# Kernel optimization log

Measured on AMD Instinct MI355X. Metric: run time of the kernel, lower is better.

Reference implementation:

```python
import jax, jax.numpy as jnp
import numpy as np

BATCH = 4096
NNZ = 32
VOCAB = 1_000_000
DIM = 64


def setup_inputs() -> dict:
    key = jax.random.key(0)
    k1, k2, k3, k4 = jax.random.split(key, 4)
    idx = jax.random.randint(k1, (BATCH, NNZ), 0, VOCAB, dtype=jnp.int32)
    vals = jax.random.uniform(k2, (BATCH, NNZ), dtype=jnp.float32)
    kernel = jax.random.normal(k3, (VOCAB, DIM), dtype=jnp.float32)
    bias = jax.random.normal(k4, (DIM,), dtype=jnp.float32)
    return {"idx": idx, "vals": vals, "kernel": kernel, "bias": bias}


def reference(idx, vals, kernel, bias):
    # Sparse [B, V] x dense [V, D] matmul == weighted gather-sum (embedding bag)
    gathered = kernel[idx]                      # [B, nnz, D] irregular gather
    out = jnp.einsum("bn,bnd->bd", vals, gathered) + bias  # [B, D]
    return out
```

## Files before the change

kernel.cpp:

```cpp
#include <hip/hip_runtime.h>
#include <hip/hip_bf16.h>


#define B_BATCH 4096
#define NNZ 32
#define DIM 64
#define LANES_PER_ROW 16

__global__ __launch_bounds__(256) void sparse_embed_kernel(
    const int* __restrict__ idx,
    const float* __restrict__ vals,
    const float* __restrict__ kern,
    const float* __restrict__ bias,
    float* __restrict__ out)
{
    const int tid  = blockIdx.x * blockDim.x + threadIdx.x;
    const int row  = tid >> 4;
    const int lane = tid & 15;
    if (row >= B_BATCH) return;

    const int*   irow = idx  + row * NNZ;
    const float* vrow = vals + row * NNZ;

    float4 acc = make_float4(0.f, 0.f, 0.f, 0.f);

    #pragma unroll
    for (int n = 0; n < NNZ; ++n) {
        const int   id = irow[n];
        const float v  = vrow[n];
        const float4 k = *reinterpret_cast<const float4*>(
            kern + (size_t)id * DIM + lane * 4);
        acc.x += v * k.x;
        acc.y += v * k.y;
        acc.z += v * k.z;
        acc.w += v * k.w;
    }

    const float4 b4 = *reinterpret_cast<const float4*>(bias + lane * 4);
    acc.x += b4.x;
    acc.y += b4.y;
    acc.z += b4.z;
    acc.w += b4.w;

    *reinterpret_cast<float4*>(out + (size_t)row * DIM + lane * 4) = acc;
}

extern "C" void kernel_launch(void* const* d_in, const int* in_sizes, int n_in,
                              void* d_out, int out_size, void* d_ws, size_t ws_size,
                              hipStream_t stream) {
    const int*   idx  = (const int*)  d_in[0];
    const float* vals = (const float*)d_in[1];
    const float* kern = (const float*)d_in[2];
    const float* bias = (const float*)d_in[3];
    float* out = (float*)d_out;

    const int threads = 256;
    const int total   = B_BATCH * LANES_PER_ROW;
    const int blocks  = (total + threads - 1) / threads;

    sparse_embed_kernel<<<blocks, threads, 0, stream>>>(idx, vals, kern, bias, out);
}
```

Before: 297.2 us.

## Split each row's nnz across 8 thread segments with shared-memory reduction

Instead of 16 threads per row serially gathering all 32 embedding rows, each row now uses 128 threads in 8 segments of 4 nonzeros each. Index and value loads become vectorized int4/float4 loads, and the four gathers per thread are issued independently to raise memory-level parallelism. Partial sums go through shared memory with a block barrier and are reduced by one segment. This trades extra LDS traffic, a sync, and idle threads during the reduction for far more gathers in flight.

```diff
diff --git a/kernel.cpp b/kernel.cpp
--- a/kernel.cpp
+++ b/kernel.cpp
@@ -1,48 +1,61 @@
 #include <hip/hip_runtime.h>
-#include <hip/hip_bf16.h>
 
 
 #define B_BATCH 4096
 #define NNZ 32
 #define DIM 64
-#define LANES_PER_ROW 16
+#define SEG 8
+#define NPT (NNZ / SEG)
+#define ROWS_PER_BLOCK 2
+#define THREADS 256
 
-__global__ __launch_bounds__(256) void sparse_embed_kernel(
+__global__ __launch_bounds__(THREADS, 8) void sparse_embed_kernel(
     const int* __restrict__ idx,
     const float* __restrict__ vals,
     const float* __restrict__ kern,
     const float* __restrict__ bias,
     float* __restrict__ out)
 {
-    const int tid  = blockIdx.x * blockDim.x + threadIdx.x;
-    const int row  = tid >> 4;
+    __shared__ float4 part[THREADS];
+
+    const int tid  = threadIdx.x;
     const int lane = tid & 15;
-    if (row >= B_BATCH) return;
+    const int seg  = (tid >> 4) & 7;
+    const int rloc = tid >> 7;
+    const int row  = blockIdx.x * ROWS_PER_BLOCK + rloc;
 
-    const int*   irow = idx  + row * NNZ;
-    const float* vrow = vals + row * NNZ;
+    const int base = row * NNZ + seg * NPT;
+    const int4   i4 = *reinterpret_cast<const int4*>(idx + base);
+    const float4 v4 = *reinterpret_cast<const float4*>(vals + base);
 
-    float4 acc = make_float4(0.f, 0.f, 0.f, 0.f);
+    const float* kslice = kern + (size_t)lane * 4;
 
-    #pragma unroll
-    for (int n = 0; n < NNZ; ++n) {
-        const int   id = irow[n];
-        const float v  = vrow[n];
-        const float4 k = *reinterpret_cast<const float4*>(
-            kern + (size_t)id * DIM + lane * 4);
-        acc.x += v * k.x;
-        acc.y += v * k.y;
-        acc.z += v * k.z;
-        acc.w += v * k.w;
+    const float4 k0 = *reinterpret_cast<const float4*>(kslice + (size_t)i4.x * DIM);
+    const float4 k1 = *reinterpret_cast<const float4*>(kslice + (size_t)i4.y * DIM);
+    const float4 k2 = *reinterpret_cast<const float4*>(kslice + (size_t)i4.z * DIM);
+    const float4 k3 = *reinterpret_cast<const float4*>(kslice + (size_t)i4.w * DIM);
+
+    float4 acc;
+    acc.x = v4.x * k0.x; acc.y = v4.x * k0.y; acc.z = v4.x * k0.z; acc.w = v4.x * k0.w;
+    acc.x += v4.y * k1.x; acc.y += v4.y * k1.y; acc.z += v4.y * k1.z; acc.w += v4.y * k1.w;
+    acc.x += v4.z * k2.x; acc.y += v4.z * k2.y; acc.z += v4.z * k2.z; acc.w += v4.z * k2.w;
+    acc.x += v4.w * k3.x; acc.y += v4.w * k3.y; acc.z += v4.w * k3.z; acc.w += v4.w * k3.w;
+
+    part[tid] = acc;
+    __syncthreads();
+
+    if (seg == 0) {
+        const int pbase = rloc * 128 + lane;
+        float4 a = part[pbase];
+        #pragma unroll
+        for (int s = 1; s < SEG; ++s) {
+            const float4 p = part[pbase + s * 16];
+            a.x += p.x; a.y += p.y; a.z += p.z; a.w += p.w;
+        }
+        const float4 b4 = *reinterpret_cast<const float4*>(bias + lane * 4);
+        a.x += b4.x; a.y += b4.y; a.z += b4.z; a.w += b4.w;
+        *reinterpret_cast<float4*>(out + (size_t)row * DIM + lane * 4) = a;
     }
-
-    const float4 b4 = *reinterpret_cast<const float4*>(bias + lane * 4);
-    acc.x += b4.x;
-    acc.y += b4.y;
-    acc.z += b4.z;
-    acc.w += b4.w;
-
-    *reinterpret_cast<float4*>(out + (size_t)row * DIM + lane * 4) = acc;
 }
 
 extern "C" void kernel_launch(void* const* d_in, const int* in_sizes, int n_in,
@@ -54,9 +67,6 @@
     const float* bias = (const float*)d_in[3];
     float* out = (float*)d_out;
 
-    const int threads = 256;
-    const int total   = B_BATCH * LANES_PER_ROW;
-    const int blocks  = (total + threads - 1) / threads;
-
-    sparse_embed_kernel<<<blocks, threads, 0, stream>>>(idx, vals, kern, bias, out);
+    const int blocks = B_BATCH / ROWS_PER_BLOCK;
+    sparse_embed_kernel<<<blocks, THREADS, 0, stream>>>(idx, vals, kern, bias, out);
 }
```

After: 296.2 us. About the same (-0.3%).
